# Performance work log

Hardware: AMD Instinct MI355X
Metric: run time of the kernel (lower is better)

The kernel has to match this reference:

```python
import jax, jax.numpy as jnp
import numpy as np

IN_F, OUT_F = 4096, 11008
B, S = 4, 2048


def setup_inputs() -> dict:
    key = jax.random.key(0)
    k1, k2, k3, k4 = jax.random.split(key, 4)
    x = jax.random.normal(k1, (B, S, IN_F), dtype=jnp.float16)
    # int8 values in [-127, 127], carried as int32 (schema has no int8)
    int8_weights = jax.random.randint(k2, (OUT_F, IN_F), -127, 128, dtype=jnp.int32)
    # per-output-row scales: positive, small, clamped at 1e-5 like _quantize_weight
    scales = (jax.random.uniform(k3, (OUT_F, 1), dtype=jnp.float32) * 0.01 + 1e-4).astype(jnp.float16)
    bias = jax.random.normal(k4, (OUT_F,), dtype=jnp.float16)
    return {"x": x, "int8_weights": int8_weights, "scales": scales, "bias": bias}


def reference(x, int8_weights, scales, bias):
    # w8a16 GEMM: dequantize int8 weights with per-row fp16 scales, then matmul.
    x2 = x.reshape(-1, IN_F).astype(jnp.float16)            # [B*S, in]
    w = int8_weights.astype(jnp.float16) * scales            # [out, in] dequant
    out = jnp.einsum('mk,nk->mn', x2, w,
                     preferred_element_type=jnp.float16)     # [B*S, out]
    out = out + bias
    return out.reshape(B, S, OUT_F)
```

## Files before the change

### kernel.cpp

```cpp
#include <hip/hip_runtime.h>

#define M_DIM 8192
#define N_DIM 11008
#define K_DIM 4096
#define K_TILES 64

typedef __bf16 bf16x8 __attribute__((ext_vector_type(8)));
typedef float  f32x4  __attribute__((ext_vector_type(4)));
typedef int    i32x4  __attribute__((ext_vector_type(4)));
typedef unsigned short u16x8 __attribute__((ext_vector_type(8)));

__device__ __forceinline__ unsigned short f2bf_rne(float f) {
  unsigned u = __float_as_uint(f);
  u += 0x7fffu + ((u >> 16) & 1u);
  return (unsigned short)(u >> 16);
}
__device__ __forceinline__ unsigned short i2bf(int v) {
  float f = (float)v;
  return (unsigned short)(__float_as_uint(f) >> 16);
}
__device__ __forceinline__ void async_copy16(void* lds_dst, const void* g_src) {
  __builtin_amdgcn_global_load_lds(
      (const __attribute__((address_space(1))) void*)g_src,
      (__attribute__((address_space(3))) void*)lds_dst,
      16, 0, 0);
}

__global__ __launch_bounds__(256)
void dequant_w_kernel(const int* __restrict__ W, unsigned short* __restrict__ Wb) {
  const int NG = N_DIM * K_DIM / 8;
  for (int g = blockIdx.x * 256 + threadIdx.x; g < NG; g += gridDim.x * 256) {
    const int* p = W + (size_t)g * 8;
    i32x4 w0 = *(const i32x4*)p;
    i32x4 w1 = *(const i32x4*)(p + 4);
    u16x8 o;
    #pragma unroll
    for (int e = 0; e < 4; ++e) { o[e] = i2bf(w0[e]); o[e + 4] = i2bf(w1[e]); }
    *(u16x8*)(Wb + (size_t)g * 8) = o;
  }
}

__global__ __launch_bounds__(256)
void conv_x_kernel(const float* __restrict__ X, unsigned short* __restrict__ Xb) {
  const int NG = M_DIM * K_DIM / 8;
  for (int g = blockIdx.x * 256 + threadIdx.x; g < NG; g += gridDim.x * 256) {
    const float* p = X + (size_t)g * 8;
    f32x4 a0 = *(const f32x4*)p;
    f32x4 a1 = *(const f32x4*)(p + 4);
    u16x8 o;
    #pragma unroll
    for (int e = 0; e < 4; ++e) { o[e] = f2bf_rne(a0[e]); o[e + 4] = f2bf_rne(a1[e]); }
    *(u16x8*)(Xb + (size_t)g * 8) = o;
  }
}

__global__ __launch_bounds__(512, 2)
void w8a16_main_kernel(const unsigned short* __restrict__ Xb,
                       const unsigned short* __restrict__ Wb,
                       const float* __restrict__ S,
                       const float* __restrict__ Bv,
                       float*       __restrict__ O)
{
  __shared__ unsigned short sh[65536];

  const int tid  = threadIdx.x;
  const int lane = tid & 63;
  const int wid  = tid >> 6;
  const int wr   = wid >> 2;
  const int wc   = wid & 3;

  const int swz = (blockIdx.x & 7) * 172 + (blockIdx.x >> 3);
  const int bm = swz / 43, bn = swz % 43;
  const int row0 = bm * 256, col0 = bn * 256;

  f32x4 acc[8][4] = {};

  bf16x8 af[4][2];
  bf16x8 bq[2][2][2];

  const int fr   = lane & 15;
  const int fkk  = (lane >> 4) * 8;
  const int sw_r = (fr & 7) << 3;
  const int aoff0 = fr * 64 + (fkk ^ sw_r);
  const int aoff1 = fr * 64 + ((fkk + 32) ^ sw_r);
  const int boff0 = aoff0;
  const int boff1 = aoff1;

  const int ch0 = wid * 2;
  const int sr0 = ch0 * 8 + (lane >> 3);
  const int sr1 = sr0 + 8;
  const int sc0 = ((lane & 7) * 8) ^ ((sr0 & 7) << 3);
  const int sc1 = ((lane & 7) * 8) ^ ((sr1 & 7) << 3);
  const unsigned short* Xs0 = Xb + (size_t)(row0 + sr0) * K_DIM + sc0;
  const unsigned short* Xs1 = Xb + (size_t)(row0 + sr1) * K_DIM + sc1;
  const unsigned short* Ws0 = Wb + (size_t)(col0 + sr0) * K_DIM + sc0;
  const unsigned short* Ws1 = Wb + (size_t)(col0 + sr1) * K_DIM + sc1;
  const size_t HALF = (size_t)128 * K_DIM;

#define STAGE_X(st, h) do { \
    unsigned short* _d = sh + ((st) & 1) * 32768 + (h) * 8192 + ch0 * 512; \
    async_copy16(_d,       Xs0 + (size_t)(h) * HALF + (size_t)(st) * 64); \
    async_copy16(_d + 512, Xs1 + (size_t)(h) * HALF + (size_t)(st) * 64); \
  } while (0)
#define STAGE_W(st, h) do { \
    unsigned short* _d = sh + ((st) & 1) * 32768 + 16384 + (h) * 8192 + ch0 * 512; \
    async_copy16(_d,       Ws0 + (size_t)(h) * HALF + (size_t)(st) * 64); \
    async_copy16(_d + 512, Ws1 + (size_t)(h) * HALF + (size_t)(st) * 64); \
  } while (0)
#define VM(N) asm volatile("s_waitcnt vmcnt(" #N ")" ::: "memory")

#define PHASE(tt, MQ, NQ, DOA, DOB, STAGE_STMT, WAIT_STMT) do { \
    const unsigned short* Ab = sh + ((tt) & 1) * 32768; \
    const unsigned short* Bb = Ab + 16384; \
    if (DOA) { \
      _Pragma("unroll") \
      for (int ii = 0; ii < 4; ++ii) { \
        af[ii][0] = *(const bf16x8*)&Ab[(2 * (4 * (MQ) + ii) + wr) * 1024 + aoff0]; \
        af[ii][1] = *(const bf16x8*)&Ab[(2 * (4 * (MQ) + ii) + wr) * 1024 + aoff1]; \
      } \
    } \
    if (DOB) { \
      _Pragma("unroll") \
      for (int jj = 0; jj < 2; ++jj) { \
        bq[NQ][jj][0] = *(const bf16x8*)&Bb[(4 * (2 * (NQ) + jj) + wc) * 1024 + boff0]; \
        bq[NQ][jj][1] = *(const bf16x8*)&Bb[(4 * (2 * (NQ) + jj) + wc) * 1024 + boff1]; \
      } \
    } \
    STAGE_STMT; \
    WAIT_STMT; \
    __builtin_amdgcn_s_barrier(); \
    __builtin_amdgcn_s_setprio(1); \
    _Pragma("unroll") \
    for (int ii = 0; ii < 4; ++ii) \
      _Pragma("unroll") \
      for (int jj = 0; jj < 2; ++jj) { \
        acc[4*(MQ)+ii][2*(NQ)+jj] = __builtin_amdgcn_mfma_f32_16x16x32_bf16(af[ii][0], bq[NQ][jj][0], acc[4*(MQ)+ii][2*(NQ)+jj], 0, 0, 0); \
        acc[4*(MQ)+ii][2*(NQ)+jj] = __builtin_amdgcn_mfma_f32_16x16x32_bf16(af[ii][1], bq[NQ][jj][1], acc[4*(MQ)+ii][2*(NQ)+jj], 0, 0, 0); \
      } \
    __builtin_amdgcn_s_setprio(0); \
    __builtin_amdgcn_s_barrier(); \
    __builtin_amdgcn_sched_barrier(0); \
  } while (0)

  STAGE_X(0, 0); STAGE_W(0, 0); STAGE_W(0, 1); STAGE_X(0, 1);
  STAGE_X(1, 0); STAGE_W(1, 0); STAGE_W(1, 1);
  VM(10);
  __builtin_amdgcn_s_barrier();

  for (int i = 0; i < K_TILES / 2 - 1; ++i) {
    const int u = 2 * i, v = 2 * i + 1;
    PHASE(u, 0, 0, 1, 1, { STAGE_X(v, 1); },     { VM(10); });
    PHASE(u, 0, 1, 0, 1, { STAGE_X(u + 2, 0); }, { VM(10); });
    PHASE(u, 1, 1, 1, 0, { STAGE_W(u + 2, 0); }, { VM(10); });
    PHASE(u, 1, 0, 0, 0, { STAGE_W(u + 2, 1); }, { VM(10); });
    PHASE(v, 0, 0, 1, 1, { STAGE_X(u + 2, 1); }, { VM(10); });
    PHASE(v, 0, 1, 0, 1, { STAGE_X(v + 2, 0); }, { VM(10); });
    PHASE(v, 1, 1, 1, 0, { STAGE_W(v + 2, 0); }, { VM(10); });
    PHASE(v, 1, 0, 0, 0, { STAGE_W(v + 2, 1); }, { VM(10); });
  }

  {
    const int u = K_TILES - 2, v = K_TILES - 1;
    PHASE(u, 0, 0, 1, 1, { STAGE_X(v, 1); }, { VM(10); });
    PHASE(u, 0, 1, 0, 1, {},                 { VM(8);  });
    PHASE(u, 1, 1, 1, 0, {},                 {});
    PHASE(u, 1, 0, 0, 0, {},                 { VM(4);  });
    PHASE(v, 0, 0, 1, 1, {},                 { VM(2);  });
    PHASE(v, 0, 1, 0, 1, {},                 { VM(0);  });
    PHASE(v, 1, 1, 1, 0, {},                 {});
    PHASE(v, 1, 0, 0, 0, {},                 {});
  }

  const int erow = (lane >> 4) * 4;
  const int ecol = lane & 15;
  #pragma unroll
  for (int j = 0; j < 4; ++j) {
    const int ocol = col0 + (4 * j + wc) * 16 + ecol;
    const float s  = S[ocol];
    const float bb = Bv[ocol];
    #pragma unroll
    for (int ii = 0; ii < 8; ++ii) {
      const int orow = row0 + (2 * ii + wr) * 16 + erow;
      #pragma unroll
      for (int e = 0; e < 4; ++e)
        O[(size_t)(orow + e) * N_DIM + ocol] = acc[ii][j][e] * s + bb;
    }
  }
#undef PHASE
#undef VM
#undef STAGE_X
#undef STAGE_W
}

#define FB_BM 128
#define FB_BK 32
#define PITCH 40
__global__ __launch_bounds__(256)
void w8a16_fallback_kernel(const float* __restrict__ X, const int* __restrict__ W,
                           const float* __restrict__ S, const float* __restrict__ Bv,
                           float* __restrict__ O)
{
  __shared__ unsigned short As[FB_BM * PITCH];
  __shared__ unsigned short Bs[FB_BM * PITCH];
  const int tid = threadIdx.x, lane = tid & 63, wid = tid >> 6;
  const int wr = wid >> 1, wc = wid & 1;
  const int p = blockIdx.x, xcd = p & 7, seq = p >> 3;
  const int bn_idx = seq >> 3, by_idx = xcd * 8 + (seq & 7);
  const int row0 = by_idx * FB_BM, col0 = bn_idx * FB_BM;
  f32x4 acc[4][4] = {};
  const int st_row = tid >> 1, st_kc = (tid & 1) * 16;
  const float* xsrc = X + (size_t)(row0 + st_row) * K_DIM + st_kc;
  const int*   wsrc = W + (size_t)(col0 + st_row) * K_DIM + st_kc;
  unsigned short* adst = &As[st_row * PITCH + st_kc];
  unsigned short* bdst = &Bs[st_row * PITCH + st_kc];
  const int fr = lane & 15, fk = (lane >> 4) * 8;
  for (int kt = 0; kt < K_DIM; kt += FB_BK) {
    f32x4 a0 = *(const f32x4*)(xsrc + kt);
    f32x4 a1 = *(const f32x4*)(xsrc + kt + 4);
    f32x4 a2 = *(const f32x4*)(xsrc + kt + 8);
    f32x4 a3 = *(const f32x4*)(xsrc + kt + 12);
    i32x4 w0 = *(const i32x4*)(wsrc + kt);
    i32x4 w1 = *(const i32x4*)(wsrc + kt + 4);
    i32x4 w2 = *(const i32x4*)(wsrc + kt + 8);
    i32x4 w3 = *(const i32x4*)(wsrc + kt + 12);
    u16x8 pa0, pa1, pb0, pb1;
    #pragma unroll
    for (int e = 0; e < 4; ++e) {
      pa0[e] = f2bf_rne(a0[e]); pa0[e+4] = f2bf_rne(a1[e]);
      pa1[e] = f2bf_rne(a2[e]); pa1[e+4] = f2bf_rne(a3[e]);
      pb0[e] = i2bf(w0[e]);     pb0[e+4] = i2bf(w1[e]);
      pb1[e] = i2bf(w2[e]);     pb1[e+4] = i2bf(w3[e]);
    }
    __syncthreads();
    *(u16x8*)(adst) = pa0; *(u16x8*)(adst + 8) = pa1;
    *(u16x8*)(bdst) = pb0; *(u16x8*)(bdst + 8) = pb1;
    __syncthreads();
    bf16x8 af2[4], bfr[4];
    #pragma unroll
    for (int i = 0; i < 4; ++i)
      af2[i] = *(const bf16x8*)&As[(wr * 64 + i * 16 + fr) * PITCH + fk];
    #pragma unroll
    for (int j = 0; j < 4; ++j)
      bfr[j] = *(const bf16x8*)&Bs[(wc * 64 + j * 16 + fr) * PITCH + fk];
    #pragma unroll
    for (int i = 0; i < 4; ++i)
      #pragma unroll
      for (int j = 0; j < 4; ++j)
        acc[i][j] = __builtin_amdgcn_mfma_f32_16x16x32_bf16(af2[i], bfr[j], acc[i][j], 0, 0, 0);
  }
  const int erow = (lane >> 4) * 4, ecol = lane & 15;
  #pragma unroll
  for (int j = 0; j < 4; ++j) {
    const int col = col0 + wc * 64 + j * 16 + ecol;
    const float s = S[col], bb = Bv[col];
    #pragma unroll
    for (int i = 0; i < 4; ++i) {
      const int rbase = row0 + wr * 64 + i * 16 + erow;
      #pragma unroll
      for (int e = 0; e < 4; ++e)
        O[(size_t)(rbase + e) * N_DIM + col] = acc[i][j][e] * s + bb;
    }
  }
}

extern "C" void kernel_launch(void* const* d_in, const int* in_sizes, int n_in,
                              void* d_out, int out_size, void* d_ws, size_t ws_size,
                              hipStream_t stream) {
  const float* x  = (const float*)d_in[0];
  const int*   w  = (const int*)d_in[1];
  const float* sc = (const float*)d_in[2];
  const float* bi = (const float*)d_in[3];
  float* out = (float*)d_out;

  const size_t w_elems = (size_t)N_DIM * K_DIM;
  const size_t x_elems = (size_t)M_DIM * K_DIM;
  const size_t need = (w_elems + x_elems) * sizeof(unsigned short);

  if (ws_size >= need) {
    unsigned short* Wb = (unsigned short*)d_ws;
    unsigned short* Xb = Wb + w_elems;
    dequant_w_kernel<<<2048, 256, 0, stream>>>(w, Wb);
    conv_x_kernel<<<2048, 256, 0, stream>>>(x, Xb);
    const int grid = (M_DIM / 256) * (N_DIM / 256);
    w8a16_main_kernel<<<grid, 512, 0, stream>>>(Xb, Wb, sc, bi, out);
  } else {
    const int grid = (M_DIM / FB_BM) * (N_DIM / FB_BM);
    w8a16_fallback_kernel<<<grid, 256, 0, stream>>>(x, w, sc, bi, out);
  }
}
```

Measured before the change: 723.1 us.

## Split-K the tail-wave GEMM tiles across two blocks with atomic accumulation

The last 96 output tiles, which form a partial final wave, are each split into two K-halves run by separate blocks. A new kernel zeroes those output tiles beforehand, and the halves combine their results with atomicAdd; only the first half adds the bias. The aim is to shorten the tail-wave imbalance across CUs, at the cost of an extra zeroing launch and float atomics on part of the output.

Result: no change. 721.2 us (-0.3%).

```diff
diff --git a/kernel.cpp b/kernel.cpp
--- a/kernel.cpp
+++ b/kernel.cpp
@@ -4,6 +4,8 @@
 #define N_DIM 11008
 #define K_DIM 4096
 #define K_TILES 64
+#define FULL_TILES 1280
+#define NTILES 1376
 
 typedef __bf16 bf16x8 __attribute__((ext_vector_type(8)));
 typedef float  f32x4  __attribute__((ext_vector_type(4)));
@@ -54,6 +56,24 @@
   }
 }
 
+__device__ __forceinline__ void tile_coords(int tile, int& row0, int& col0) {
+  const int swz = (tile & 7) * 172 + (tile >> 3);
+  const int bm = swz / 43, bn = swz % 43;
+  row0 = bm * 256; col0 = bn * 256;
+}
+
+__global__ __launch_bounds__(256)
+void zero_partial_kernel(float* __restrict__ O) {
+  int row0, col0;
+  tile_coords(FULL_TILES + blockIdx.x, row0, col0);
+  const int tidx = threadIdx.x;
+  for (int r = 0; r < 256; ++r) {
+    float* rowp = O + (size_t)(row0 + r) * N_DIM + col0;
+    for (int c4 = tidx; c4 < 64; c4 += 256)
+      *(f32x4*)(rowp + c4 * 4) = f32x4{0.f, 0.f, 0.f, 0.f};
+  }
+}
+
 __global__ __launch_bounds__(512, 2)
 void w8a16_main_kernel(const unsigned short* __restrict__ Xb,
                        const unsigned short* __restrict__ Wb,
@@ -69,9 +89,19 @@
   const int wr   = wid >> 2;
   const int wc   = wid & 3;
 
-  const int swz = (blockIdx.x & 7) * 172 + (blockIdx.x >> 3);
-  const int bm = swz / 43, bn = swz % 43;
-  const int row0 = bm * 256, col0 = bn * 256;
+  const int bid = blockIdx.x;
+  int tile, half, nkt, partial;
+  if (bid < FULL_TILES) { tile = bid; half = 0; nkt = K_TILES; partial = 0; }
+  else {
+    const int idx = bid - FULL_TILES;
+    tile = FULL_TILES + (idx >> 1);
+    half = idx & 1;
+    nkt  = K_TILES / 2;
+    partial = 1;
+  }
+  int row0, col0;
+  tile_coords(tile, row0, col0);
+  const size_t kbase = (size_t)half * (K_TILES / 2) * 64;
 
   f32x4 acc[8][4] = {};
 
@@ -91,10 +121,10 @@
   const int sr1 = sr0 + 8;
   const int sc0 = ((lane & 7) * 8) ^ ((sr0 & 7) << 3);
   const int sc1 = ((lane & 7) * 8) ^ ((sr1 & 7) << 3);
-  const unsigned short* Xs0 = Xb + (size_t)(row0 + sr0) * K_DIM + sc0;
-  const unsigned short* Xs1 = Xb + (size_t)(row0 + sr1) * K_DIM + sc1;
-  const unsigned short* Ws0 = Wb + (size_t)(col0 + sr0) * K_DIM + sc0;
-  const unsigned short* Ws1 = Wb + (size_t)(col0 + sr1) * K_DIM + sc1;
+  const unsigned short* Xs0 = Xb + (size_t)(row0 + sr0) * K_DIM + kbase + sc0;
+  const unsigned short* Xs1 = Xb + (size_t)(row0 + sr1) * K_DIM + kbase + sc1;
+  const unsigned short* Ws0 = Wb + (size_t)(col0 + sr0) * K_DIM + kbase + sc0;
+  const unsigned short* Ws1 = Wb + (size_t)(col0 + sr1) * K_DIM + kbase + sc1;
   const size_t HALF = (size_t)128 * K_DIM;
 
 #define STAGE_X(st, h) do { \
@@ -147,7 +177,7 @@
   VM(10);
   __builtin_amdgcn_s_barrier();
 
-  for (int i = 0; i < K_TILES / 2 - 1; ++i) {
+  for (int i = 0; i < nkt / 2 - 1; ++i) {
     const int u = 2 * i, v = 2 * i + 1;
     PHASE(u, 0, 0, 1, 1, { STAGE_X(v, 1); },     { VM(10); });
     PHASE(u, 0, 1, 0, 1, { STAGE_X(u + 2, 0); }, { VM(10); });
@@ -160,7 +190,7 @@
   }
 
   {
-    const int u = K_TILES - 2, v = K_TILES - 1;
+    const int u = nkt - 2, v = nkt - 1;
     PHASE(u, 0, 0, 1, 1, { STAGE_X(v, 1); }, { VM(10); });
     PHASE(u, 0, 1, 0, 1, {},                 { VM(8);  });
     PHASE(u, 1, 1, 1, 0, {},                 {});
@@ -177,13 +207,17 @@
   for (int j = 0; j < 4; ++j) {
     const int ocol = col0 + (4 * j + wc) * 16 + ecol;
     const float s  = S[ocol];
-    const float bb = Bv[ocol];
+    const float bb = (partial && half == 1) ? 0.0f : Bv[ocol];
     #pragma unroll
     for (int ii = 0; ii < 8; ++ii) {
       const int orow = row0 + (2 * ii + wr) * 16 + erow;
       #pragma unroll
-      for (int e = 0; e < 4; ++e)
-        O[(size_t)(orow + e) * N_DIM + ocol] = acc[ii][j][e] * s + bb;
+      for (int e = 0; e < 4; ++e) {
+        const float v = acc[ii][j][e] * s + bb;
+        float* dst = &O[(size_t)(orow + e) * N_DIM + ocol];
+        if (partial) atomicAdd(dst, v);
+        else         *dst = v;
+      }
     }
   }
 #undef PHASE
@@ -279,9 +313,10 @@
   if (ws_size >= need) {
     unsigned short* Wb = (unsigned short*)d_ws;
     unsigned short* Xb = Wb + w_elems;
+    zero_partial_kernel<<<NTILES - FULL_TILES, 256, 0, stream>>>(out);
     dequant_w_kernel<<<2048, 256, 0, stream>>>(w, Wb);
     conv_x_kernel<<<2048, 256, 0, stream>>>(x, Xb);
-    const int grid = (M_DIM / 256) * (N_DIM / 256);
+    const int grid = FULL_TILES + 2 * (NTILES - FULL_TILES);
     w8a16_main_kernel<<<grid, 512, 0, stream>>>(Xb, Wb, sc, bi, out);
   } else {
     const int grid = (M_DIM / FB_BM) * (N_DIM / FB_BM);
```
